# Optimization experiments

Measured on AMD Instinct MI355X. Metric: run time of the kernel, lower is better.

The kernel has to match this reference:

```python
import jax, jax.numpy as jnp
import numpy as np

B, L, D = 128, 196, 512
T = 20
V, E, H, A = 10000, 256, 512, 512


def setup_inputs() -> dict:
    key = jax.random.key(0)
    ks = jax.random.split(key, 20)
    s = lambda *sh: 0.02
    inp = {
        "a": jax.random.normal(ks[0], (B, L, D), jnp.float32),
        "captions": jax.random.randint(ks[1], (B, T), 0, V),
        "lengths": jnp.full((B,), T, dtype=jnp.int64),
        "embed_W": jax.random.normal(ks[2], (V, E), jnp.float32) * 0.02,
        "Wa": jax.random.normal(ks[3], (D, A), jnp.float32) * 0.02,
        "Wh": jax.random.normal(ks[4], (H, A), jnp.float32) * 0.02,
        "Wc": jax.random.normal(ks[5], (H, A), jnp.float32) * 0.02,
        "v": jax.random.normal(ks[6], (A,), jnp.float32) * 0.02,
        "beta_W": jax.random.normal(ks[7], (H, 1), jnp.float32) * 0.02,
        "beta_b": jnp.zeros((1,), jnp.float32),
        "W_ih": jax.random.normal(ks[8], (E + D, 4 * H), jnp.float32) * 0.02,
        "W_hh": jax.random.normal(ks[9], (H, 4 * H), jnp.float32) * 0.02,
        "b_ih": jnp.zeros((4 * H,), jnp.float32),
        "b_hh": jnp.zeros((4 * H,), jnp.float32),
        "fc_W": jax.random.normal(ks[10], (H, V), jnp.float32) * 0.02,
        "fc_b": jnp.zeros((V,), jnp.float32),
        "initW_h": jax.random.normal(ks[11], (D, H), jnp.float32) * 0.02,
        "initb_h": jnp.zeros((H,), jnp.float32),
        "initW_c": jax.random.normal(ks[12], (D, H), jnp.float32) * 0.02,
        "initb_c": jnp.zeros((H,), jnp.float32),
    }
    return inp


def _decode(a, captions, embed_W, Wa, Wh, Wc, v, beta_W, beta_b,
            W_ih, W_hh, b_ih, b_hh, fc_W, fc_b,
            initW_h, initb_h, initW_c, initb_c):
    # dropout layers are treated as identity (eval mode) for a deterministic reference
    emb = embed_W[captions]                       # (B, T, E)
    mean_ctx = a.mean(axis=1)                     # (B, D)
    h0 = jnp.tanh(mean_ctx @ initW_h + initb_h)   # (B, H)
    c0 = jnp.tanh(mean_ctx @ initW_c + initb_c)
    wa = a @ Wa                                   # (B, L, A), hoisted (invariant over t)
    Hd = h0.shape[-1]

    def step(carry, x_t):
        h, c, prev_h = carry
        # dual additive attention: scores from annotations + h + prev_h (context_input)
        score = jnp.tanh(wa + (h @ Wh)[:, None, :] + (prev_h @ Wc)[:, None, :])  # (B,L,A)
        e = score @ v                                                            # (B,L)
        alpha = jax.nn.softmax(e, axis=1)
        beta = jax.nn.sigmoid(h @ beta_W + beta_b)                               # (B,1)
        ctx = beta * jnp.einsum('bl,bld->bd', alpha, a)                          # (B,D)
        # LSTMCell
        x = jnp.concatenate([x_t, ctx], axis=1)                                  # (B,E+D)
        gates = x @ W_ih + b_ih + h @ W_hh + b_hh                                # (B,4H)
        i, f, g, o = jnp.split(gates, 4, axis=1)
        c_new = jax.nn.sigmoid(f) * c + jax.nn.sigmoid(i) * jnp.tanh(g)
        h_new = jax.nn.sigmoid(o) * jnp.tanh(c_new)
        logits_t = h_new @ fc_W + fc_b                                           # (B,V)
        return (h_new, c_new, h_new), (logits_t, alpha)

    xs = jnp.swapaxes(emb[:, :T - 1, :], 0, 1)    # (T-1, B, E) time-major
    _, (logits_t, alphas_t) = jax.lax.scan(step, (h0, c0, h0), xs)
    # all lengths == T: pack_padded_sequence(batch_first=True).data is time-major flatten
    packed_logits = logits_t.reshape((T - 1) * a.shape[0], -1)                   # ((T-1)*B, V)
    alphas = jnp.swapaxes(alphas_t, 0, 1)                                        # (B, T-1, L)
    return packed_logits, alphas


def reference(a, captions, lengths, embed_W, Wa, Wh, Wc, v, beta_W, beta_b,
              W_ih, W_hh, b_ih, b_hh, fc_W, fc_b,
              initW_h, initb_h, initW_c, initb_c):
    return _decode(a, captions, embed_W, Wa, Wh, Wc, v, beta_W, beta_b,
                   W_ih, W_hh, b_ih, b_hh, fc_W, fc_b,
                   initW_h, initb_h, initW_c, initb_c)
```

## Files before the change

kernel.cpp:

```cpp
#include <hip/hip_runtime.h>
#include <hip/hip_bf16.h>
#include <math.h>

#define B_ 128
#define L_ 196
#define D_ 512
#define T_ 20
#define V_ 10000
#define E_ 256
#define H_ 512
#define A_ 512
#define TM1 19
#define ROWS (TM1*B_)
#define G4H 2048
#define KCAT 1024
#define LH 98

typedef unsigned short ushort_t;
typedef __attribute__((ext_vector_type(8))) short bf16x8;
typedef __attribute__((ext_vector_type(4))) float f32x4;

__device__ __forceinline__ float fast_tanh(float x){
    float ax = fabsf(x);
    float e = __expf(-2.f*ax);
    float r = __builtin_amdgcn_rcpf(1.f + e);
    return copysignf((1.f - e)*r, x);
}
__device__ __forceinline__ float sigmoidf_(float x){
    return __builtin_amdgcn_rcpf(1.f + __expf(-x));
}
__device__ __forceinline__ ushort_t f2b(float f){
    union{float f; unsigned u;} x; x.f = f;
    unsigned r = x.u + 0x7fffu + ((x.u>>16)&1u);
    return (ushort_t)(r>>16);
}
__device__ __forceinline__ float b2f(ushort_t h){
    union{unsigned u; float f;} x; x.u = ((unsigned)h)<<16;
    return x.f;
}
__device__ __forceinline__ float b2f_lo(unsigned u){ union{unsigned u; float f;} x; x.u = u<<16; return x.f; }
__device__ __forceinline__ float b2f_hi(unsigned u){ union{unsigned u; float f;} x; x.u = u & 0xffff0000u; return x.f; }

template<int OUT_BF16, int HAS_BIAS, int NT, int SWZ>
__global__ __launch_bounds__(256)
void gemm_mfma(const ushort_t* __restrict__ A, int lda,
               const ushort_t* __restrict__ BT, int ldb,
               void* __restrict__ Cout, int ldc,
               int N, int K, const float* __restrict__ bias)
{
    __shared__ ushort_t As[128*32];
    __shared__ ushort_t Bs[128*32];
    int bm, bn;
    if (SWZ){
        int bid = blockIdx.x;
        int swz = (bid & 7)*190 + (bid >> 3);
        int mt = swz % 19, nt = swz / 19;
        if (nt >= 79) return;
        bm = mt*128; bn = nt*128;
    } else {
        bm = blockIdx.y * 128; bn = blockIdx.x * 128;
    }
    const int tid = threadIdx.x;
    const int lane = tid & 63;
    const int wave = tid >> 6;
    const int wm = (wave >> 1) * 64;
    const int wn = (wave & 1) * 64;
    const int lrow = lane & 15;
    const int lk8  = (lane >> 4) * 8;
    const int srow = tid >> 2;
    const int skq  = ((tid & 3) * 8) ^ ((srow & 3) << 3);
    const int skq0 = (tid & 3) * 8;

    f32x4 acc[4][4];
    #pragma unroll
    for (int i=0;i<4;i++)
        #pragma unroll
        for (int j=0;j<4;j++) acc[i][j] = (f32x4){0.f,0.f,0.f,0.f};

    const ushort_t* Abase = A  + (size_t)(bm+srow)*lda + skq0;
    const ushort_t* Bbase = BT + (size_t)(bn+srow)*ldb + skq0;

    for (int k0 = 0; k0 < K; k0 += 32) {
        int4 a0 = *(const int4*)(Abase + k0);
        int4 a1 = *(const int4*)(Abase + (size_t)64*lda + k0);
        int4 b0 = *(const int4*)(Bbase + k0);
        int4 b1 = *(const int4*)(Bbase + (size_t)64*ldb + k0);
        __syncthreads();
        *(int4*)&As[srow*32 + skq]      = a0;
        *(int4*)&As[(srow+64)*32 + skq] = a1;
        *(int4*)&Bs[srow*32 + skq]      = b0;
        *(int4*)&Bs[(srow+64)*32 + skq] = b1;
        __syncthreads();
        bf16x8 af[4], bfr[4];
        #pragma unroll
        for (int i=0;i<4;i++){
            int r = wm + i*16 + lrow;
            af[i]  = *(bf16x8*)&As[r*32 + (lk8 ^ ((r & 3) << 3))];
        }
        #pragma unroll
        for (int j=0;j<4;j++){
            int r = wn + j*16 + lrow;
            bfr[j] = *(bf16x8*)&Bs[r*32 + (lk8 ^ ((r & 3) << 3))];
        }
        #pragma unroll
        for (int i=0;i<4;i++)
            #pragma unroll
            for (int j=0;j<4;j++)
                acc[i][j] = __builtin_amdgcn_mfma_f32_16x16x32_bf16(af[i], bfr[j], acc[i][j], 0, 0, 0);
    }

    const int rq = (lane >> 4) * 4;
    #pragma unroll
    for (int j=0;j<4;j++){
        int col = bn + wn + j*16 + lrow;
        if (col >= N) continue;
        float bv = HAS_BIAS ? bias[col] : 0.f;
        #pragma unroll
        for (int i=0;i<4;i++){
            #pragma unroll
            for (int q=0;q<4;q++){
                int row = bm + wm + i*16 + rq + q;
                float v = acc[i][j][q] + bv;
                if (OUT_BF16) ((ushort_t*)Cout)[(size_t)row*ldc + col] = f2b(v);
                else if (NT)  __builtin_nontemporal_store(v, &((float*)Cout)[(size_t)row*ldc + col]);
                else          ((float*)Cout)[(size_t)row*ldc + col] = v;
            }
        }
    }
}

__global__ __launch_bounds__(256) void gemm64t(const float* __restrict__ A, int lda,
                       const float* __restrict__ Bm, int ldb,
                       float* __restrict__ C, int ldc, const float* __restrict__ bias)
{
    __shared__ float As[16][65];
    __shared__ float Bs[16][65];
    int bm = blockIdx.y*64, bn = blockIdx.x*64;
    int tid = threadIdx.x;
    int tx = tid & 15, ty = tid >> 4;
    float acc[4][4] = {};
    for (int k0 = 0; k0 < D_; k0 += 16) {
        {
            int r  = tid >> 2;
            int kq = (tid & 3) * 4;
            float4 va = *(const float4*)(A + (size_t)(bm+r)*lda + k0 + kq);
            As[kq+0][r]=va.x; As[kq+1][r]=va.y; As[kq+2][r]=va.z; As[kq+3][r]=va.w;
        }
        {
            int kk = tid >> 4;
            int nq = (tid & 15) * 4;
            float4 vb = *(const float4*)(Bm + (size_t)(k0+kk)*ldb + bn + nq);
            Bs[kk][nq+0]=vb.x; Bs[kk][nq+1]=vb.y; Bs[kk][nq+2]=vb.z; Bs[kk][nq+3]=vb.w;
        }
        __syncthreads();
        #pragma unroll
        for (int k = 0; k < 16; ++k) {
            float a0[4], b0[4];
            #pragma unroll
            for (int i=0;i<4;i++) a0[i] = As[k][ty*4+i];
            #pragma unroll
            for (int j=0;j<4;j++) b0[j] = Bs[k][tx*4+j];
            #pragma unroll
            for (int i=0;i<4;i++)
                #pragma unroll
                for (int j=0;j<4;j++)
                    acc[i][j] = fmaf(a0[i], b0[j], acc[i][j]);
        }
        __syncthreads();
    }
    #pragma unroll
    for (int i=0;i<4;i++){
        int row = bm + ty*4 + i;
        #pragma unroll
        for (int j=0;j<4;j++){
            int col = bn + tx*4 + j;
            C[(size_t)row*ldc + col] = fast_tanh(acc[i][j] + bias[col]);
        }
    }
}

__global__ void transpose_cvt(const float* __restrict__ src, const float* __restrict__ src2,
                              int lds_, int Ksz, int Nsz,
                              ushort_t* __restrict__ dst, int ldk, int koff)
{
    __shared__ float t[32][33];
    int n0 = blockIdx.x*32, k0 = blockIdx.y*32;
    int tx = threadIdx.x & 31, ty = threadIdx.x >> 5;
    #pragma unroll
    for (int kk = ty; kk < 32; kk += 8){
        int k = k0 + kk, n = n0 + tx;
        float v = 0.f;
        if (k < Ksz && n < Nsz){
            v = src[(size_t)k*lds_ + n];
            if (src2) v += src2[(size_t)k*lds_ + n];
        }
        t[kk][tx] = v;
    }
    __syncthreads();
    #pragma unroll
    for (int nn = ty; nn < 32; nn += 8){
        int n = n0 + nn, k = k0 + tx;
        if (k < Ksz) dst[(size_t)n*ldk + koff + k] = f2b(t[tx][nn]);
    }
}

__global__ void bias4h_k(const float* __restrict__ b_ih, const float* __restrict__ b_hh,
                         float* __restrict__ bias4h, unsigned* __restrict__ ebar){
    int i = blockIdx.x*blockDim.x + threadIdx.x;
    if (i < G4H) bias4h[i] = b_ih[i] + b_hh[i];
    if (i < B_) ebar[i] = 0u;
}

__global__ __launch_bounds__(256) void mean_cvt_k(const float* __restrict__ a, ushort_t* __restrict__ a_b,
                                                  float* __restrict__ mc){
    int idx = blockIdx.x*256 + threadIdx.x;
    int b = idx >> 9, d = idx & 511;
    const float* p = a + (size_t)b*L_*D_ + d;
    ushort_t* q = a_b + (size_t)b*L_*D_ + d;
    float s = 0.f;
    for (int l=0;l<L_;l++){ float v = p[(size_t)l*D_]; s += v; q[(size_t)l*D_] = f2b(v); }
    mc[idx] = s * (1.f/(float)L_);
}

__global__ void gather_emb(const int* __restrict__ captions, const float* __restrict__ embW,
                           ushort_t* __restrict__ xemb){
    int i = blockIdx.x;
    int t = i / B_, b = i - t*B_;
    int cap = captions[b*T_ + t];
    float4 v = ((const float4*)(embW + (size_t)cap*E_))[threadIdx.x];
    ushort_t r[4] = {f2b(v.x),f2b(v.y),f2b(v.z),f2b(v.w)};
    *(uint2*)(xemb + (size_t)i*E_ + threadIdx.x*4) = *(uint2*)r;
}

__global__ void cvt_h0_k(const float* __restrict__ h0f, ushort_t* __restrict__ xcat){
    int idx = blockIdx.x*blockDim.x + threadIdx.x;
    int b = idx >> 9, j = idx & 511;
    xcat[(size_t)b*KCAT + D_ + j] = f2b(h0f[idx]);
}

__device__ __forceinline__ void hw_mfma_phase(const ushort_t* hls, const ushort_t* __restrict__ WhcT,
                                              float* __restrict__ hW, int b, int j){
    int lane = j & 63, wave = j >> 6;
    int wn = wave * 64;
    int col16 = lane & 15;
    int khi = (lane >> 4) * 8;
    bool a_on = (col16 == 0);
    f32x4 acc[4];
    #pragma unroll
    for (int f=0;f<4;f++) acc[f] = (f32x4){0.f,0.f,0.f,0.f};
    for (int kk=0; kk<16; kk++){
        bf16x8 af = (bf16x8){0,0,0,0,0,0,0,0};
        if (a_on) af = *(const bf16x8*)&hls[kk*32 + khi];
        #pragma unroll
        for (int f=0;f<4;f++){
            bf16x8 bf = *(const bf16x8*)(WhcT + (size_t)(wn + f*16 + col16)*512 + kk*32 + khi);
            acc[f] = __builtin_amdgcn_mfma_f32_16x16x32_bf16(af, bf, acc[f], 0, 0, 0);
        }
    }
    if (lane < 16){
        #pragma unroll
        for (int f=0;f<4;f++) hW[b*512 + wn + f*16 + lane] = acc[f][0];
    }
}

__global__ __launch_bounds__(512) void hw0_k(const ushort_t* __restrict__ xcat,
                                             const ushort_t* __restrict__ WhcT, float* __restrict__ hW){
    int b = blockIdx.x, j = threadIdx.x;
    __shared__ ushort_t hls[512];
    hls[j] = xcat[(size_t)b*KCAT + D_ + j];
    __syncthreads();
    hw_mfma_phase(hls, WhcT, hW, b, j);
}

__global__ __launch_bounds__(512) void attn_k(const ushort_t* __restrict__ wa,
                        const ushort_t* __restrict__ a_b,
                        const float* __restrict__ hW,
                        const float* __restrict__ v,
                        const float* __restrict__ beta_W, const float* __restrict__ beta_b,
                        ushort_t* __restrict__ xcat, float* __restrict__ alphas_out,
                        float* __restrict__ ebuf, unsigned* __restrict__ ebar, int t)
{
    const int b = blockIdx.x, half = blockIdx.y;
    const int tid = threadIdx.x;
    const int lane = tid & 63, wave = tid >> 6;
    __shared__ float red[512];
    __shared__ float al_s[224];
    __shared__ float part[2][256];

    const float* hp = hW + b*512 + lane*8;
    float4 hw0 = *(const float4*)hp, hw1 = *(const float4*)(hp+4);
    const float* vp = v + lane*8;
    float4 v0 = *(const float4*)vp, v1 = *(const float4*)(vp+4);

    const int l0 = half*LH;
    for (int r = wave; r < LH; r += 8){
        int4 raw = *(const int4*)(wa + (((size_t)(b*L_ + l0 + r))<<9) + lane*8);
        const unsigned* u = (const unsigned*)&raw;
        float s;
        s  = fast_tanh(b2f_lo(u[0]) + hw0.x)*v0.x;
        s += fast_tanh(b2f_hi(u[0]) + hw0.y)*v0.y;
        s += fast_tanh(b2f_lo(u[1]) + hw0.z)*v0.z;
        s += fast_tanh(b2f_hi(u[1]) + hw0.w)*v0.w;
        s += fast_tanh(b2f_lo(u[2]) + hw1.x)*v1.x;
        s += fast_tanh(b2f_hi(u[2]) + hw1.y)*v1.y;
        s += fast_tanh(b2f_lo(u[3]) + hw1.z)*v1.z;
        s += fast_tanh(b2f_hi(u[3]) + hw1.w)*v1.w;
        #pragma unroll
        for (int off=32; off; off>>=1) s += __shfl_down(s, off);
        if (lane==0) ebuf[b*L_ + l0 + r] = s;
    }
    __syncthreads();
    if (tid == 0){
        __threadfence();
        atomicAdd(&ebar[b], 1u);
        const unsigned tgt = 2u*(unsigned)(t+1);
        while (__hip_atomic_load(&ebar[b], __ATOMIC_ACQUIRE, __HIP_MEMORY_SCOPE_AGENT) < tgt)
            __builtin_amdgcn_s_sleep(1);
    }
    __syncthreads();
    float ev = (tid < L_) ? ebuf[b*L_ + tid] : -3.0e38f;
    red[tid] = ev; __syncthreads();
    #pragma unroll
    for (int s=256; s; s>>=1){ if (tid<s) red[tid] = fmaxf(red[tid], red[tid+s]); __syncthreads(); }
    float m = red[0]; __syncthreads();
    float pr = (tid < L_) ? __expf(ev - m) : 0.f;
    red[tid] = pr; __syncthreads();
    #pragma unroll
    for (int s=256; s; s>>=1){ if (tid<s) red[tid] += red[tid+s]; __syncthreads(); }
    float inv = 1.f / red[0];
    __syncthreads();
    if (tid < L_) al_s[tid] = pr*inv;
    if (tid >= l0 && tid < l0 + LH)
        __builtin_nontemporal_store(pr*inv, alphas_out + (size_t)b*TM1*L_ + (size_t)t*L_ + tid);
    float dv = b2f(xcat[(size_t)b*KCAT + D_ + tid]) * beta_W[tid];
    red[tid] = dv; __syncthreads();
    #pragma unroll
    for (int s=256; s; s>>=1){ if (tid<s) red[tid] += red[tid+s]; __syncthreads(); }
    float beta = sigmoidf_(red[0] + beta_b[0]);
    __syncthreads();
    const int d  = half*256 + (tid & 255);
    const int lr = tid >> 8;
    const ushort_t* pa = a_b + (((size_t)(b*L_ + lr*LH))<<9) + d;
    float s0 = 0.f;
    #pragma unroll 7
    for (int i=0; i<LH; ++i) s0 = fmaf(al_s[lr*LH + i], b2f(pa[(size_t)i*512]), s0);
    part[lr][tid & 255] = s0;
    __syncthreads();
    if (tid < 256)
        xcat[(size_t)b*KCAT + half*256 + tid] = f2b(beta*(part[0][tid] + part[1][tid]));
}

__global__ __launch_bounds__(256) void gates_k(const ushort_t* __restrict__ xcat,
                        const ushort_t* __restrict__ WcatT, float* __restrict__ gp){
    __shared__ ushort_t As[128*32];
    __shared__ ushort_t Bs[64*32];
    const int bn = blockIdx.x*64;
    const int ks = blockIdx.y;
    const int tid = threadIdx.x;
    const int lane = tid & 63, wave = tid >> 6;
    const int wm = wave*32;
    const int lrow = lane & 15;
    const int lk8 = (lane >> 4) * 8;
    f32x4 acc[2][4];
    #pragma unroll
    for (int i=0;i<2;i++)
        #pragma unroll
        for (int j=0;j<4;j++) acc[i][j] = (f32x4){0.f,0.f,0.f,0.f};

    for (int kk = 0; kk < 8; ++kk){
        int k0 = ks*256 + kk*32;
        int c0 = 2*tid;
        int r0 = c0 >> 2,  kq0 = (c0 & 3)*8;
        int r1 = (c0+1) >> 2, kq1 = ((c0+1) & 3)*8;
        int4 a0 = *(const int4*)(xcat + (size_t)r0*KCAT + k0 + kq0);
        int4 a1 = *(const int4*)(xcat + (size_t)r1*KCAT + k0 + kq1);
        int rb = tid >> 2, kqb = (tid & 3)*8;
        int4 b0 = *(const int4*)(WcatT + (size_t)(bn+rb)*KCAT + k0 + kqb);
        __syncthreads();
        *(int4*)&As[r0*32 + kq0] = a0;
        *(int4*)&As[r1*32 + kq1] = a1;
        *(int4*)&Bs[rb*32 + kqb] = b0;
        __syncthreads();
        bf16x8 af[2], bfr[4];
        #pragma unroll
        for (int i=0;i<2;i++) af[i] = *(bf16x8*)&As[(wm + i*16 + lrow)*32 + lk8];
        #pragma unroll
        for (int j=0;j<4;j++) bfr[j] = *(bf16x8*)&Bs[(j*16 + lrow)*32 + lk8];
        #pragma unroll
        for (int i=0;i<2;i++)
            #pragma unroll
            for (int j=0;j<4;j++)
                acc[i][j] = __builtin_amdgcn_mfma_f32_16x16x32_bf16(af[i], bfr[j], acc[i][j], 0, 0, 0);
    }
    const int rq = (lane >> 4) * 4;
    #pragma unroll
    for (int i=0;i<2;i++){
        #pragma unroll
        for (int j=0;j<4;j++){
            int gcol = bn + j*16 + lrow;
            #pragma unroll
            for (int q=0;q<4;q++){
                int grow = wm + i*16 + rq + q;
                gp[((size_t)(ks*B_ + grow))*G4H + gcol] = acc[i][j][q];
            }
        }
    }
}

__global__ __launch_bounds__(512) void lstm_hw_k(const float* __restrict__ gp, const float* __restrict__ embWih,
                       float* __restrict__ cbuf, ushort_t* __restrict__ xcat, ushort_t* __restrict__ Hall,
                       const ushort_t* __restrict__ WhcT, float* __restrict__ hW, int t){
    int b = blockIdx.x, j = threadIdx.x;
    __shared__ ushort_t hls[512];
    float gi, gf, gg, go;
    {
        const float* eb = embWih + ((size_t)(t*B_ + b))*G4H;
        gi = eb[j]; gf = eb[H_+j]; gg = eb[2*H_+j]; go = eb[3*H_+j];
    }
    #pragma unroll
    for (int ks=0; ks<4; ks++){
        const float* g = gp + ((size_t)(ks*B_ + b))*G4H;
        gi += g[j]; gf += g[H_+j]; gg += g[2*H_+j]; go += g[3*H_+j];
    }
    float ig = sigmoidf_(gi), fg = sigmoidf_(gf);
    float g2 = fast_tanh(gg), og = sigmoidf_(go);
    float c = fg*cbuf[b*H_+j] + ig*g2;
    float h = og*fast_tanh(c);
    cbuf[b*H_+j] = c;
    ushort_t hb = f2b(h);
    xcat[(size_t)b*KCAT + D_ + j] = hb;
    Hall[((size_t)t*B_ + b)*H_ + j] = hb;
    hls[j] = hb;
    __syncthreads();
    hw_mfma_phase(hls, WhcT, hW, b, j);
}

extern "C" void kernel_launch(void* const* d_in, const int* in_sizes, int n_in,
                              void* d_out, int out_size, void* d_ws, size_t ws_size,
                              hipStream_t stream) {
    const float* a      = (const float*)d_in[0];
    const int*   caps   = (const int*)  d_in[1];
    const float* embW   = (const float*)d_in[3];
    const float* Wa     = (const float*)d_in[4];
    const float* Wh     = (const float*)d_in[5];
    const float* Wc     = (const float*)d_in[6];
    const float* v      = (const float*)d_in[7];
    const float* beta_W = (const float*)d_in[8];
    const float* beta_b = (const float*)d_in[9];
    const float* W_ih   = (const float*)d_in[10];
    const float* W_hh   = (const float*)d_in[11];
    const float* b_ih   = (const float*)d_in[12];
    const float* b_hh   = (const float*)d_in[13];
    const float* fc_W   = (const float*)d_in[14];
    const float* fc_b   = (const float*)d_in[15];
    const float* iWh    = (const float*)d_in[16];
    const float* ibh    = (const float*)d_in[17];
    const float* iWc    = (const float*)d_in[18];
    const float* ibc    = (const float*)d_in[19];

    float* out    = (float*)d_out;
    float* alphas = out + (size_t)ROWS*V_;

    char* ob = (char*)d_out;
    ushort_t* wa_b   = (ushort_t*)(ob);
    ushort_t* a_b    = (ushort_t*)(ob + 25690112);
    float*    embWih = (float*)   (ob + 51380224);

    char* wb = (char*)d_ws;
    float* mean_ctx = (float*)(wb);
    float* cbuf     = (float*)(wb + 262144);
    float* h0f      = (float*)(wb + 524288);
    float* hWbuf    = (float*)(wb + 786432);
    float* ebuf     = (float*)(wb + 1048576);
    float* bias4h   = (float*)(wb + 1179648);
    float* gp       = (float*)(wb + 1187840);
    ushort_t* xcat_b = (ushort_t*)(wb + 5382144);
    ushort_t* xemb_b = (ushort_t*)(wb + 5644288);
    ushort_t* Hall   = (ushort_t*)(wb + 6889472);
    ushort_t* WaT    = (ushort_t*)(wb + 9379840);
    ushort_t* WhcT   = (ushort_t*)(wb + 9904128);
    ushort_t* WihT   = (ushort_t*)(wb + 10428416);
    ushort_t* WcatT  = (ushort_t*)(wb + 11476992);
    ushort_t* fcWT   = (ushort_t*)(wb + 15671296);
    unsigned* ebar   = (unsigned*)(wb + 26025984);

    bias4h_k<<<8, 256, 0, stream>>>(b_ih, b_hh, bias4h, ebar);
    transpose_cvt<<<dim3(16,16), 256, 0, stream>>>(Wa, nullptr, A_, D_, A_, WaT, 512, 0);
    transpose_cvt<<<dim3(16,16), 256, 0, stream>>>(Wh, Wc,      A_, H_, A_, WhcT, 512, 0);
    transpose_cvt<<<dim3(64,8),  256, 0, stream>>>(W_ih, nullptr, G4H, E_, G4H, WihT, 256, 0);
    transpose_cvt<<<dim3(64,16), 256, 0, stream>>>(W_ih + (size_t)E_*G4H, nullptr, G4H, D_, G4H, WcatT, KCAT, 0);
    transpose_cvt<<<dim3(64,16), 256, 0, stream>>>(W_hh, nullptr, G4H, H_, G4H, WcatT, KCAT, 512);
    transpose_cvt<<<dim3(316,16),256, 0, stream>>>(fc_W, nullptr, V_, H_, V_, fcWT, 512, 0);
    mean_cvt_k<<<256, 256, 0, stream>>>(a, a_b, mean_ctx);
    gather_emb<<<ROWS, 64, 0, stream>>>(caps, embW, xemb_b);

    gemm64t<<<dim3(8,2), 256, 0, stream>>>(mean_ctx, D_, iWh, H_, h0f, H_, ibh);
    gemm64t<<<dim3(8,2), 256, 0, stream>>>(mean_ctx, D_, iWc, H_, cbuf, H_, ibc);
    cvt_h0_k<<<256, 256, 0, stream>>>(h0f, xcat_b);
    hw0_k<<<B_, 512, 0, stream>>>(xcat_b, WhcT, hWbuf);

    gemm_mfma<1,0,0,0><<<dim3(4,196), 256, 0, stream>>>(a_b, D_, WaT, D_, wa_b, A_, A_, D_, nullptr);
    gemm_mfma<0,1,0,0><<<dim3(16,19), 256, 0, stream>>>(xemb_b, E_, WihT, E_, embWih, G4H, G4H, E_, bias4h);

    for (int t = 0; t < TM1; ++t){
        attn_k<<<dim3(B_,2), 512, 0, stream>>>(wa_b, a_b, hWbuf, v, beta_W, beta_b,
                                               xcat_b, alphas, ebuf, ebar, t);
        gates_k<<<dim3(32,4), 256, 0, stream>>>(xcat_b, WcatT, gp);
        lstm_hw_k<<<B_, 512, 0, stream>>>(gp, embWih, cbuf, xcat_b, Hall, WhcT, hWbuf, t);
    }
    gemm_mfma<0,1,1,1><<<dim3(1520), 256, 0, stream>>>(Hall, H_, fcWT, H_, out, V_, V_, H_, fc_b);
}
```

Measured before the change: 1.141 ms.

## Fuse LSTM cell update into attention kernel and merge setup launches

Moves the LSTM cell update and the h·[Wh+Wc] projection for step t-1 into the start of the per-step attention kernel. The hW matvec is split across the two half-blocks and synchronized with the existing per-batch spin barrier. This cuts the per-step launch count from three to two, and a final small kernel finishes the last LSTM step. The gates GEMM split-K is doubled from 4 to 8 to raise parallelism, at the cost of summing more partials. Setup kernels are also consolidated: six transposes become one multi-job kernel, the bias init folds into mean_cvt, the two init GEMMs share one launch, and the h0 conversion merges with its projection.

```diff
diff --git a/kernel.cpp b/kernel.cpp
--- a/kernel.cpp
+++ b/kernel.cpp
@@ -129,10 +129,14 @@
     }
 }
 
-__global__ __launch_bounds__(256) void gemm64t(const float* __restrict__ A, int lda,
-                       const float* __restrict__ Bm, int ldb,
-                       float* __restrict__ C, int ldc, const float* __restrict__ bias)
+__global__ __launch_bounds__(256) void gemm64t2(const float* __restrict__ A, int lda,
+                       const float* __restrict__ B0, const float* __restrict__ B1, int ldb,
+                       float* __restrict__ C0, float* __restrict__ C1, int ldc,
+                       const float* __restrict__ bias0, const float* __restrict__ bias1)
 {
+    const float* Bm  = blockIdx.z ? B1 : B0;
+    float* C         = blockIdx.z ? C1 : C0;
+    const float* bias= blockIdx.z ? bias1 : bias0;
     __shared__ float As[16][65];
     __shared__ float Bs[16][65];
     int bm = blockIdx.y*64, bn = blockIdx.x*64;
@@ -179,20 +183,25 @@
     }
 }
 
-__global__ void transpose_cvt(const float* __restrict__ src, const float* __restrict__ src2,
-                              int lds_, int Ksz, int Nsz,
-                              ushort_t* __restrict__ dst, int ldk, int koff)
-{
+struct TJob { const float* src; const float* src2; ushort_t* dst;
+              int lds, Ksz, Nsz, koff, ldk, nx, nblk; };
+struct TJobs { TJob j[6]; };
+
+__global__ __launch_bounds__(256) void combo_trans_k(TJobs J){
     __shared__ float t[32][33];
-    int n0 = blockIdx.x*32, k0 = blockIdx.y*32;
+    int bid = blockIdx.x;
+    int ji = 0;
+    while (bid >= J.j[ji].nblk){ bid -= J.j[ji].nblk; ji++; }
+    const TJob jb = J.j[ji];
+    int n0 = (bid % jb.nx)*32, k0 = (bid / jb.nx)*32;
     int tx = threadIdx.x & 31, ty = threadIdx.x >> 5;
     #pragma unroll
     for (int kk = ty; kk < 32; kk += 8){
         int k = k0 + kk, n = n0 + tx;
         float v = 0.f;
-        if (k < Ksz && n < Nsz){
-            v = src[(size_t)k*lds_ + n];
-            if (src2) v += src2[(size_t)k*lds_ + n];
+        if (k < jb.Ksz && n < jb.Nsz){
+            v = jb.src[(size_t)k*jb.lds + n];
+            if (jb.src2) v += jb.src2[(size_t)k*jb.lds + n];
         }
         t[kk][tx] = v;
     }
@@ -200,19 +209,19 @@
     #pragma unroll
     for (int nn = ty; nn < 32; nn += 8){
         int n = n0 + nn, k = k0 + tx;
-        if (k < Ksz) dst[(size_t)n*ldk + koff + k] = f2b(t[tx][nn]);
-    }
-}
-
-__global__ void bias4h_k(const float* __restrict__ b_ih, const float* __restrict__ b_hh,
-                         float* __restrict__ bias4h, unsigned* __restrict__ ebar){
-    int i = blockIdx.x*blockDim.x + threadIdx.x;
-    if (i < G4H) bias4h[i] = b_ih[i] + b_hh[i];
-    if (i < B_) ebar[i] = 0u;
+        if (k < jb.Ksz) jb.dst[(size_t)n*jb.ldk + jb.koff + k] = f2b(t[tx][nn]);
+    }
 }
 
 __global__ __launch_bounds__(256) void mean_cvt_k(const float* __restrict__ a, ushort_t* __restrict__ a_b,
-                                                  float* __restrict__ mc){
+                                                  float* __restrict__ mc,
+                                                  const float* __restrict__ b_ih, const float* __restrict__ b_hh,
+                                                  float* __restrict__ bias4h, unsigned* __restrict__ ebar){
+    if (blockIdx.x == 256){
+        for (int k = threadIdx.x; k < G4H; k += 256) bias4h[k] = b_ih[k] + b_hh[k];
+        if (threadIdx.x < B_) ebar[threadIdx.x] = 0u;
+        return;
+    }
     int idx = blockIdx.x*256 + threadIdx.x;
     int b = idx >> 9, d = idx & 511;
     const float* p = a + (size_t)b*L_*D_ + d;
@@ -232,15 +241,18 @@
     *(uint2*)(xemb + (size_t)i*E_ + threadIdx.x*4) = *(uint2*)r;
 }
 
-__global__ void cvt_h0_k(const float* __restrict__ h0f, ushort_t* __restrict__ xcat){
-    int idx = blockIdx.x*blockDim.x + threadIdx.x;
-    int b = idx >> 9, j = idx & 511;
-    xcat[(size_t)b*KCAT + D_ + j] = f2b(h0f[idx]);
-}
-
-__device__ __forceinline__ void hw_mfma_phase(const ushort_t* hls, const ushort_t* __restrict__ WhcT,
-                                              float* __restrict__ hW, int b, int j){
-    int lane = j & 63, wave = j >> 6;
+__global__ __launch_bounds__(512) void hw0cvt_k(const float* __restrict__ h0f,
+                        const ushort_t* __restrict__ WhcT,
+                        ushort_t* __restrict__ xcat, float* __restrict__ hWp){
+    int b = blockIdx.x, tid = threadIdx.x;
+    int lane = tid & 63, wave = tid >> 6;
+    __shared__ ushort_t hls[512];
+    float hv = h0f[b*H_ + tid];
+    ushort_t hb = f2b(hv);
+    xcat[(size_t)b*KCAT + D_ + tid] = hb;
+    hls[tid] = hb;
+    hWp[(size_t)(b*2+1)*512 + tid] = 0.f;
+    __syncthreads();
     int wn = wave * 64;
     int col16 = lane & 15;
     int khi = (lane >> 4) * 8;
@@ -259,61 +271,113 @@
     }
     if (lane < 16){
         #pragma unroll
-        for (int f=0;f<4;f++) hW[b*512 + wn + f*16 + lane] = acc[f][0];
-    }
-}
-
-__global__ __launch_bounds__(512) void hw0_k(const ushort_t* __restrict__ xcat,
-                                             const ushort_t* __restrict__ WhcT, float* __restrict__ hW){
-    int b = blockIdx.x, j = threadIdx.x;
-    __shared__ ushort_t hls[512];
-    hls[j] = xcat[(size_t)b*KCAT + D_ + j];
-    __syncthreads();
-    hw_mfma_phase(hls, WhcT, hW, b, j);
-}
-
-__global__ __launch_bounds__(512) void attn_k(const ushort_t* __restrict__ wa,
+        for (int f=0;f<4;f++) hWp[(size_t)(b*2+0)*512 + wn + f*16 + lane] = acc[f][0];
+    }
+}
+
+__global__ __launch_bounds__(512) void mega2_k(const ushort_t* __restrict__ wa,
                         const ushort_t* __restrict__ a_b,
-                        const float* __restrict__ hW,
                         const float* __restrict__ v,
                         const float* __restrict__ beta_W, const float* __restrict__ beta_b,
-                        ushort_t* __restrict__ xcat, float* __restrict__ alphas_out,
-                        float* __restrict__ ebuf, unsigned* __restrict__ ebar, int t)
+                        const ushort_t* __restrict__ WhcT,
+                        const float* __restrict__ gp, const float* __restrict__ embWih,
+                        float* __restrict__ cbuf, float* __restrict__ hWp,
+                        ushort_t* __restrict__ xcat, ushort_t* __restrict__ Hall,
+                        float* __restrict__ alphas_out, float* __restrict__ ebuf,
+                        unsigned* __restrict__ ebar, int t)
 {
     const int b = blockIdx.x, half = blockIdx.y;
     const int tid = threadIdx.x;
     const int lane = tid & 63, wave = tid >> 6;
+    __shared__ ushort_t hls[256];
     __shared__ float red[512];
     __shared__ float al_s[224];
     __shared__ float part[2][256];
 
-    const float* hp = hW + b*512 + lane*8;
-    float4 hw0 = *(const float4*)hp, hw1 = *(const float4*)(hp+4);
-    const float* vp = v + lane*8;
-    float4 v0 = *(const float4*)vp, v1 = *(const float4*)(vp+4);
-
-    const int l0 = half*LH;
-    for (int r = wave; r < LH; r += 8){
-        int4 raw = *(const int4*)(wa + (((size_t)(b*L_ + l0 + r))<<9) + lane*8);
-        const unsigned* u = (const unsigned*)&raw;
-        float s;
-        s  = fast_tanh(b2f_lo(u[0]) + hw0.x)*v0.x;
-        s += fast_tanh(b2f_hi(u[0]) + hw0.y)*v0.y;
-        s += fast_tanh(b2f_lo(u[1]) + hw0.z)*v0.z;
-        s += fast_tanh(b2f_hi(u[1]) + hw0.w)*v0.w;
-        s += fast_tanh(b2f_lo(u[2]) + hw1.x)*v1.x;
-        s += fast_tanh(b2f_hi(u[2]) + hw1.y)*v1.y;
-        s += fast_tanh(b2f_lo(u[3]) + hw1.z)*v1.z;
-        s += fast_tanh(b2f_hi(u[3]) + hw1.w)*v1.w;
-        #pragma unroll
-        for (int off=32; off; off>>=1) s += __shfl_down(s, off);
-        if (lane==0) ebuf[b*L_ + l0 + r] = s;
+    if (t > 0){
+        if (tid < 256){
+            const int j = half*256 + tid;
+            const float* eb = embWih + ((size_t)((t-1)*B_ + b))*G4H;
+            float gi = eb[j], gf = eb[H_+j], gg = eb[2*H_+j], go = eb[3*H_+j];
+            #pragma unroll
+            for (int ks=0; ks<8; ks++){
+                const float* g = gp + ((size_t)(ks*B_ + b))*G4H;
+                gi += g[j]; gf += g[H_+j]; gg += g[2*H_+j]; go += g[3*H_+j];
+            }
+            float ig = sigmoidf_(gi), fg = sigmoidf_(gf);
+            float g2 = fast_tanh(gg), og = sigmoidf_(go);
+            float c = fg*cbuf[b*H_+j] + ig*g2;
+            float h = og*fast_tanh(c);
+            cbuf[b*H_+j] = c;
+            ushort_t hb = f2b(h);
+            xcat[(size_t)b*KCAT + D_ + j] = hb;
+            Hall[((size_t)(t-1)*B_ + b)*H_ + j] = hb;
+            hls[tid] = hb;
+        }
+        __syncthreads();
+        int wn = wave * 64;
+        int col16 = lane & 15;
+        int khi = (lane >> 4) * 8;
+        bool a_on = (col16 == 0);
+        f32x4 acc[4];
+        #pragma unroll
+        for (int f=0;f<4;f++) acc[f] = (f32x4){0.f,0.f,0.f,0.f};
+        #pragma unroll
+        for (int kk=0; kk<8; kk++){
+            bf16x8 af = (bf16x8){0,0,0,0,0,0,0,0};
+            if (a_on) af = *(const bf16x8*)&hls[kk*32 + khi];
+            #pragma unroll
+            for (int f=0;f<4;f++){
+                bf16x8 bf = *(const bf16x8*)(WhcT + (size_t)(wn + f*16 + col16)*512 + half*256 + kk*32 + khi);
+                acc[f] = __builtin_amdgcn_mfma_f32_16x16x32_bf16(af, bf, acc[f], 0, 0, 0);
+            }
+        }
+        if (lane < 16){
+            #pragma unroll
+            for (int f=0;f<4;f++) hWp[(size_t)(b*2+half)*512 + wn + f*16 + lane] = acc[f][0];
+        }
     }
     __syncthreads();
     if (tid == 0){
         __threadfence();
         atomicAdd(&ebar[b], 1u);
-        const unsigned tgt = 2u*(unsigned)(t+1);
+        const unsigned tgt = 2u*(unsigned)(2*t+1);
+        while (__hip_atomic_load(&ebar[b], __ATOMIC_ACQUIRE, __HIP_MEMORY_SCOPE_AGENT) < tgt)
+            __builtin_amdgcn_s_sleep(1);
+    }
+    __syncthreads();
+    {
+        const float* hp0 = hWp + (size_t)(b*2+0)*512 + lane*8;
+        const float* hp1 = hWp + (size_t)(b*2+1)*512 + lane*8;
+        float4 p00 = *(const float4*)hp0, p01 = *(const float4*)(hp0+4);
+        float4 p10 = *(const float4*)hp1, p11 = *(const float4*)(hp1+4);
+        float4 hw0 = make_float4(p00.x+p10.x, p00.y+p10.y, p00.z+p10.z, p00.w+p10.w);
+        float4 hw1 = make_float4(p01.x+p11.x, p01.y+p11.y, p01.z+p11.z, p01.w+p11.w);
+        const float* vp = v + lane*8;
+        float4 v0 = *(const float4*)vp, v1 = *(const float4*)(vp+4);
+        const int l0 = half*LH;
+        for (int r = wave; r < LH; r += 8){
+            int4 raw = *(const int4*)(wa + (((size_t)(b*L_ + l0 + r))<<9) + lane*8);
+            const unsigned* u = (const unsigned*)&raw;
+            float s;
+            s  = fast_tanh(b2f_lo(u[0]) + hw0.x)*v0.x;
+            s += fast_tanh(b2f_hi(u[0]) + hw0.y)*v0.y;
+            s += fast_tanh(b2f_lo(u[1]) + hw0.z)*v0.z;
+            s += fast_tanh(b2f_hi(u[1]) + hw0.w)*v0.w;
+            s += fast_tanh(b2f_lo(u[2]) + hw1.x)*v1.x;
+            s += fast_tanh(b2f_hi(u[2]) + hw1.y)*v1.y;
+            s += fast_tanh(b2f_lo(u[3]) + hw1.z)*v1.z;
+            s += fast_tanh(b2f_hi(u[3]) + hw1.w)*v1.w;
+            #pragma unroll
+            for (int off=32; off; off>>=1) s += __shfl_down(s, off);
+            if (lane==0) ebuf[b*L_ + l0 + r] = s;
+        }
+    }
+    __syncthreads();
+    if (tid == 0){
+        __threadfence();
+        atomicAdd(&ebar[b], 1u);
+        const unsigned tgt = 2u*(unsigned)(2*t+2);
         while (__hip_atomic_load(&ebar[b], __ATOMIC_ACQUIRE, __HIP_MEMORY_SCOPE_AGENT) < tgt)
             __builtin_amdgcn_s_sleep(1);
     }
@@ -330,6 +394,7 @@
     float inv = 1.f / red[0];
     __syncthreads();
     if (tid < L_) al_s[tid] = pr*inv;
+    const int l0 = half*LH;
     if (tid >= l0 && tid < l0 + LH)
         __builtin_nontemporal_store(pr*inv, alphas_out + (size_t)b*TM1*L_ + (size_t)t*L_ + tid);
     float dv = b2f(xcat[(size_t)b*KCAT + D_ + tid]) * beta_W[tid];
@@ -367,8 +432,8 @@
         #pragma unroll
         for (int j=0;j<4;j++) acc[i][j] = (f32x4){0.f,0.f,0.f,0.f};
 
-    for (int kk = 0; kk < 8; ++kk){
-        int k0 = ks*256 + kk*32;
+    for (int kk = 0; kk < 4; ++kk){
+        int k0 = ks*128 + kk*32;
         int c0 = 2*tid;
         int r0 = c0 >> 2,  kq0 = (c0 & 3)*8;
         int r1 = (c0+1) >> 2, kq1 = ((c0+1) & 3)*8;
@@ -407,18 +472,13 @@
     }
 }
 
-__global__ __launch_bounds__(512) void lstm_hw_k(const float* __restrict__ gp, const float* __restrict__ embWih,
-                       float* __restrict__ cbuf, ushort_t* __restrict__ xcat, ushort_t* __restrict__ Hall,
-                       const ushort_t* __restrict__ WhcT, float* __restrict__ hW, int t){
+__global__ __launch_bounds__(512) void lstmfin_k(const float* __restrict__ gp, const float* __restrict__ embWih,
+                       const float* __restrict__ cbuf, ushort_t* __restrict__ Hall){
     int b = blockIdx.x, j = threadIdx.x;
-    __shared__ ushort_t hls[512];
-    float gi, gf, gg, go;
-    {
-        const float* eb = embWih + ((size_t)(t*B_ + b))*G4H;
-        gi = eb[j]; gf = eb[H_+j]; gg = eb[2*H_+j]; go = eb[3*H_+j];
-    }
-    #pragma unroll
-    for (int ks=0; ks<4; ks++){
+    const float* eb = embWih + ((size_t)(18*B_ + b))*G4H;
+    float gi = eb[j], gf = eb[H_+j], gg = eb[2*H_+j], go = eb[3*H_+j];
+    #pragma unroll
+    for (int ks=0; ks<8; ks++){
         const float* g = gp + ((size_t)(ks*B_ + b))*G4H;
         gi += g[j]; gf += g[H_+j]; gg += g[2*H_+j]; go += g[3*H_+j];
     }
@@ -426,13 +486,7 @@
     float g2 = fast_tanh(gg), og = sigmoidf_(go);
     float c = fg*cbuf[b*H_+j] + ig*g2;
     float h = og*fast_tanh(c);
-    cbuf[b*H_+j] = c;
-    ushort_t hb = f2b(h);
-    xcat[(size_t)b*KCAT + D_ + j] = hb;
-    Hall[((size_t)t*B_ + b)*H_ + j] = hb;
-    hls[j] = hb;
-    __syncthreads();
-    hw_mfma_phase(hls, WhcT, hW, b, j);
+    Hall[((size_t)18*B_ + b)*H_ + j] = f2b(h);
 }
 
 extern "C" void kernel_launch(void* const* d_in, const int* in_sizes, int n_in,
@@ -470,43 +524,42 @@
     float* mean_ctx = (float*)(wb);
     float* cbuf     = (float*)(wb + 262144);
     float* h0f      = (float*)(wb + 524288);
-    float* hWbuf    = (float*)(wb + 786432);
-    float* ebuf     = (float*)(wb + 1048576);
-    float* bias4h   = (float*)(wb + 1179648);
-    float* gp       = (float*)(wb + 1187840);
-    ushort_t* xcat_b = (ushort_t*)(wb + 5382144);
-    ushort_t* xemb_b = (ushort_t*)(wb + 5644288);
-    ushort_t* Hall   = (ushort_t*)(wb + 6889472);
-    ushort_t* WaT    = (ushort_t*)(wb + 9379840);
-    ushort_t* WhcT   = (ushort_t*)(wb + 9904128);
-    ushort_t* WihT   = (ushort_t*)(wb + 10428416);
-    ushort_t* WcatT  = (ushort_t*)(wb + 11476992);
-    ushort_t* fcWT   = (ushort_t*)(wb + 15671296);
-    unsigned* ebar   = (unsigned*)(wb + 26025984);
-
-    bias4h_k<<<8, 256, 0, stream>>>(b_ih, b_hh, bias4h, ebar);
-    transpose_cvt<<<dim3(16,16), 256, 0, stream>>>(Wa, nullptr, A_, D_, A_, WaT, 512, 0);
-    transpose_cvt<<<dim3(16,16), 256, 0, stream>>>(Wh, Wc,      A_, H_, A_, WhcT, 512, 0);
-    transpose_cvt<<<dim3(64,8),  256, 0, stream>>>(W_ih, nullptr, G4H, E_, G4H, WihT, 256, 0);
-    transpose_cvt<<<dim3(64,16), 256, 0, stream>>>(W_ih + (size_t)E_*G4H, nullptr, G4H, D_, G4H, WcatT, KCAT, 0);
-    transpose_cvt<<<dim3(64,16), 256, 0, stream>>>(W_hh, nullptr, G4H, H_, G4H, WcatT, KCAT, 512);
-    transpose_cvt<<<dim3(316,16),256, 0, stream>>>(fc_W, nullptr, V_, H_, V_, fcWT, 512, 0);
-    mean_cvt_k<<<256, 256, 0, stream>>>(a, a_b, mean_ctx);
+    float* hWp      = (float*)(wb + 786432);
+    float* ebuf     = (float*)(wb + 1310720);
+    float* bias4h   = (float*)(wb + 1413120);
+    unsigned* ebar  = (unsigned*)(wb + 1421312);
+    float* gp       = (float*)(wb + 1422336);
+    ushort_t* xcat_b = (ushort_t*)(wb + 9810944);
+    ushort_t* xemb_b = (ushort_t*)(wb + 10073088);
+    ushort_t* Hall   = (ushort_t*)(wb + 11318272);
+    ushort_t* WaT    = (ushort_t*)(wb + 13808640);
+    ushort_t* WhcT   = (ushort_t*)(wb + 14332928);
+    ushort_t* WihT   = (ushort_t*)(wb + 14857216);
+    ushort_t* WcatT  = (ushort_t*)(wb + 15905792);
+    ushort_t* fcWT   = (ushort_t*)(wb + 20100096);
+
+    TJobs J;
+    J.j[0] = { Wa,   nullptr, WaT,  512, 512, 512,  0,   512,  16, 256 };
+    J.j[1] = { Wh,   Wc,      WhcT, 512, 512, 512,  0,   512,  16, 256 };
+    J.j[2] = { W_ih, nullptr, WihT, G4H, 256, G4H,  0,   256,  64, 512 };
+    J.j[3] = { W_ih + (size_t)E_*G4H, nullptr, WcatT, G4H, 512, G4H, 0,   KCAT, 64, 1024 };
+    J.j[4] = { W_hh, nullptr, WcatT, G4H, 512, G4H,  512, KCAT, 64, 1024 };
+    J.j[5] = { fc_W, nullptr, fcWT, V_,  512, V_,   0,   512,  316, 5056 };
+    combo_trans_k<<<8128, 256, 0, stream>>>(J);
+    mean_cvt_k<<<257, 256, 0, stream>>>(a, a_b, mean_ctx, b_ih, b_hh, bias4h, ebar);
     gather_emb<<<ROWS, 64, 0, stream>>>(caps, embW, xemb_b);
-
-    gemm64t<<<dim3(8,2), 256, 0, stream>>>(mean_ctx, D_, iWh, H_, h0f, H_, ibh);
-    gemm64t<<<dim3(8,2), 256, 0, stream>>>(mean_ctx, D_, iWc, H_, cbuf, H_, ibc);
-    cvt_h0_k<<<256, 256, 0, stream>>>(h0f, xcat_b);
-    hw0_k<<<B_, 512, 0, stream>>>(xcat_b, WhcT, hWbuf);
-
+    gemm64t2<<<dim3(8,2,2), 256, 0, stream>>>(mean_ctx, D_, iWh, iWc, H_, h0f, cbuf, H_, ibh, ibc);
+    hw0cvt_k<<<B_, 512, 0, stream>>>(h0f, WhcT, xcat_b, hWp);
     gemm_mfma<1,0,0,0><<<dim3(4,196), 256, 0, stream>>>(a_b, D_, WaT, D_, wa_b, A_, A_, D_, nullptr);
     gemm_mfma<0,1,0,0><<<dim3(16,19), 256, 0, stream>>>(xemb_b, E_, WihT, E_, embWih, G4H, G4H, E_, bias4h);
 
     for (int t = 0; t < TM1; ++t){
-        attn_k<<<dim3(B_,2), 512, 0, stream>>>(wa_b, a_b, hWbuf, v, beta_W, beta_b,
-                                               xcat_b, alphas, ebuf, ebar, t);
-        gates_k<<<dim3(32,4), 256, 0, stream>>>(xcat_b, WcatT, gp);
-        lstm_hw_k<<<B_, 512, 0, stream>>>(gp, embWih, cbuf, xcat_b, Hall, WhcT, hWbuf, t);
-    }
+        mega2_k<<<dim3(B_,2), 512, 0, stream>>>(wa_b, a_b, v, beta_W, beta_b, WhcT,
+                                                gp, embWih, cbuf, hWp, xcat_b, Hall,
+                                                alphas, ebuf, ebar, t);
+        gates_k<<<dim3(32,8), 256, 0, stream>>>(xcat_b, WcatT, gp);
+    }
+    lstmfin_k<<<B_, 512, 0, stream>>>(gp, embWih, cbuf, Hall);
+
     gemm_mfma<0,1,1,1><<<dim3(1520), 256, 0, stream>>>(Hall, H_, fcWT, H_, out, V_, V_, H_, fc_b);
 }
```

Measured after the change: 1.054 ms. 7.6% less time.
